# Kernel tuning notes

Measured on AMD Instinct MI355X. Metric: run time of the kernel, lower is better.

## Reference

```python
import jax, jax.numpy as jnp
import numpy as np

N_NODES = 50000


def gcn_conv(h, W, b, src, dst, n_nodes):
    # PyG GCNConv: h' = D^{-1/2} (A + I) D^{-1/2} (h @ W) + b
    h = h @ W  # [N, out]
    deg = jax.ops.segment_sum(jnp.ones_like(dst, dtype=h.dtype), dst, num_segments=n_nodes)
    dinv = jnp.where(deg > 0, jax.lax.rsqrt(deg), 0.0)  # [N]
    norm = dinv[src] * dinv[dst]  # [E]
    msg = h[src] * norm[:, None]  # [E, out]
    out = jax.ops.segment_sum(msg, dst, num_segments=n_nodes)
    return out + b


def setup_inputs() -> dict:
    key = jax.random.key(0)
    ks = jax.random.split(key, 12)
    N, E, P, D, H = N_NODES, 1600000, 200000, 128, 128
    s = lambda fan_in: 1.0 / np.sqrt(fan_in)
    return {
        "x": jax.random.normal(ks[0], (N, D), dtype=jnp.float32),
        "edge_index": jax.random.randint(ks[1], (2, E), 0, N, dtype=jnp.int32),
        "drug_pairs": jax.random.randint(ks[2], (P, 2), 0, N, dtype=jnp.int32),
        "W1": jax.random.normal(ks[3], (D, H), dtype=jnp.float32) * s(D),
        "b1": jnp.zeros((H,), dtype=jnp.float32),
        "W2": jax.random.normal(ks[4], (H, H), dtype=jnp.float32) * s(H),
        "b2": jnp.zeros((H,), dtype=jnp.float32),
        "Wh1": jax.random.normal(ks[5], (2 * H, H), dtype=jnp.float32) * s(2 * H),
        "bh1": jnp.zeros((H,), dtype=jnp.float32),
        "Wh2": jax.random.normal(ks[6], (H, 1), dtype=jnp.float32) * s(H),
        "bh2": jnp.zeros((1,), dtype=jnp.float32),
    }


def reference(x, edge_index, drug_pairs, W1, b1, W2, b2, Wh1, bh1, Wh2, bh2):
    n = x.shape[0]
    # add self-loops once (GCNConv default add_self_loops=True)
    loop = jnp.arange(n, dtype=edge_index.dtype)
    src = jnp.concatenate([edge_index[0], loop])
    dst = jnp.concatenate([edge_index[1], loop])

    h = jax.nn.relu(gcn_conv(x, W1, b1, src, dst, n))  # dropout = identity (eval)
    h = jax.nn.relu(gcn_conv(h, W2, b2, src, dst, n))

    combined = jnp.concatenate([h[drug_pairs[:, 0]], h[drug_pairs[:, 1]]], axis=1)  # [P, 2H]
    out = jax.nn.relu(combined @ Wh1 + bh1) @ Wh2 + bh2  # [P, 1]
    return out
```

## Files before the change

### kernel.cpp

```cpp
#include <hip/hip_runtime.h>
#include <hip/hip_fp16.h>


#define BSH 9
#define BSZ (1 << BSH)
#define MSB 4096
#define XPAD 132

typedef __attribute__((ext_vector_type(8))) short bf16x8;
typedef __attribute__((ext_vector_type(4))) float f32x4;

__device__ __forceinline__ float4 h4_to_f4(uint2 u) {
  float2 fa = __half22float2(*(__half2*)&u.x);
  float2 fb = __half22float2(*(__half2*)&u.y);
  return make_float4(fa.x, fa.y, fb.x, fb.y);
}

__global__ __launch_bounds__(256) void k_zero_i32(int* __restrict__ p, int n) {
  int i = blockIdx.x * 256 + threadIdx.x;
  if (i < n) p[i] = 0;
}

__global__ __launch_bounds__(256) void k_bucket_hist(const int* __restrict__ dst,
                                                     int* __restrict__ gcnt,
                                                     int e, int kb) {
  __shared__ int h[128];
  int tid = threadIdx.x;
  if (tid < kb) h[tid] = 0;
  __syncthreads();
  int stride = gridDim.x * 256;
  for (int i = blockIdx.x * 256 + tid; i < e; i += stride) {
    int d = __builtin_nontemporal_load(&dst[i]);
    atomicAdd(&h[d >> BSH], 1);
  }
  __syncthreads();
  if (tid < kb) atomicAdd(&gcnt[tid], h[tid]);
}

__global__ __launch_bounds__(128) void k_bucket_scan(const int* __restrict__ gcnt,
                                                     int* __restrict__ gbase,
                                                     int* __restrict__ gcur,
                                                     int kb) {
  __shared__ int ws[2];
  int t = threadIdx.x;
  int lane = t & 63, w = t >> 6;
  int v = (t < kb) ? gcnt[t] : 0;
  int orig = v;
#pragma unroll
  for (int o = 1; o < 64; o <<= 1) {
    int u = __shfl_up(v, o, 64);
    if (lane >= o) v += u;
  }
  if (lane == 63) ws[w] = v;
  __syncthreads();
  int ex = ((w == 1) ? ws[0] : 0) + v - orig;
  if (t < kb) { gbase[t] = ex; gcur[t] = ex; }
  if (t == kb - 1) gbase[kb] = ex + orig;
}

__global__ __launch_bounds__(256) void k_multisplit(const int* __restrict__ src,
                                                    const int* __restrict__ dst,
                                                    int* __restrict__ gcur,
                                                    int* __restrict__ tmp,
                                                    int e, int kb) {
  __shared__ int h[128], base[128];
  int tid = threadIdx.x;
  if (tid < kb) h[tid] = 0;
  __syncthreads();
  int i0 = blockIdx.x * MSB + tid;
  int d[16], rk[16];
#pragma unroll
  for (int u = 0; u < 16; ++u) {
    int i = i0 + u * 256;
    if (i < e) {
      d[u] = __builtin_nontemporal_load(&dst[i]);
      rk[u] = atomicAdd(&h[d[u] >> BSH], 1);
    }
  }
  __syncthreads();
  if (tid < kb && h[tid] > 0) base[tid] = atomicAdd(&gcur[tid], h[tid]);
  __syncthreads();
#pragma unroll
  for (int u = 0; u < 16; ++u) {
    int i = i0 + u * 256;
    if (i < e) {
      int s = __builtin_nontemporal_load(&src[i]);
      tmp[base[d[u] >> BSH] + rk[u]] = ((d[u] & (BSZ - 1)) << 16) | s;
    }
  }
}

__global__ __launch_bounds__(512) void k_bucket_build(
    const int* __restrict__ tmp, const int* __restrict__ gbase,
    int* __restrict__ rowptr, float* __restrict__ dinv,
    unsigned short* __restrict__ colarr, int n, int kb, int e) {
  __shared__ int dl[BSZ], cl[BSZ], ws[8];
  int t = threadIdx.x, b = blockIdx.x;
  int s0 = gbase[b], s1 = gbase[b + 1];
  dl[t] = 0;
  __syncthreads();
  for (int j = s0 + t; j < s1; j += 512)
    atomicAdd(&dl[((unsigned)tmp[j]) >> 16], 1);
  __syncthreads();
  int lane = t & 63, w = t >> 6;
  int v = dl[t], orig = v;
#pragma unroll
  for (int o = 1; o < 64; o <<= 1) {
    int u = __shfl_up(v, o, 64);
    if (lane >= o) v += u;
  }
  if (lane == 63) ws[w] = v;
  __syncthreads();
  if (t == 0) {
    int a = 0;
#pragma unroll
    for (int k = 0; k < 8; ++k) { int x = ws[k]; ws[k] = a; a += x; }
  }
  __syncthreads();
  int ex = ws[w] + v - orig;
  cl[t] = ex;
  int node = (b << BSH) + t;
  if (node < n) {
    rowptr[node] = s0 + ex;
    dinv[node] = rsqrtf((float)(orig + 1));
  }
  if (b == kb - 1 && t == 0) rowptr[n] = e;
  __syncthreads();
  for (int j = s0 + t; j < s1; j += 512) {
    int p = tmp[j];
    int r = atomicAdd(&cl[((unsigned)p) >> 16], 1);
    colarr[s0 + r] = (unsigned short)(p & 0xFFFF);
  }
}

__device__ __forceinline__ void split8(const float* v, bf16x8& hi, bf16x8& lo) {
#pragma unroll
  for (int j = 0; j < 8; ++j) {
    unsigned u = __float_as_uint(v[j]);
    hi[j] = (short)(u >> 16);
    float lf = v[j] - __uint_as_float(u & 0xffff0000u);
    lo[j] = (short)(__float_as_uint(lf) >> 16);
  }
}

__global__ __launch_bounds__(256) void k_prep_w(
    const float* __restrict__ W1, const float* __restrict__ W2,
    const float* __restrict__ Wh1, short* __restrict__ fragH,
    short* __restrict__ fragL) {
  int g = blockIdx.x * 256 + threadIdx.x;
  if (g >= 4 * 2048) return;
  int w = g >> 11;
  int rem = g & 2047;
  int lane = rem & 63;
  int ts = rem >> 6;
  int t = ts >> 2, s = ts & 3;
  int n = (t << 4) + (lane & 15);
  int k0 = s * 32 + (lane >> 4) * 8;
  const float* W = (w == 0) ? W1 : (w == 1) ? W2 : (w == 2) ? Wh1 : (Wh1 + 128 * 128);
  short h[8], l[8];
#pragma unroll
  for (int j = 0; j < 8; ++j) {
    float x = W[(k0 + j) * 128 + n];
    unsigned u = __float_as_uint(x);
    h[j] = (short)(u >> 16);
    float lf = x - __uint_as_float(u & 0xffff0000u);
    l[j] = (short)(__float_as_uint(lf) >> 16);
  }
  ((int4*)fragH)[g] = *(int4*)h;
  ((int4*)fragL)[g] = *(int4*)l;
}

__global__ __launch_bounds__(256) void k_gemm_mfma(
    const float* __restrict__ X, const short* __restrict__ fragH,
    const short* __restrict__ fragL, const float* __restrict__ rowscale,
    __half* __restrict__ C16, int n) {
  __shared__ float sX[64 * XPAD];
  int tid = threadIdx.x;
  int row0 = blockIdx.x * 64;
  const float2* X2 = (const float2*)(X + (size_t)row0 * 128);
#pragma unroll
  for (int it = 0; it < 16; ++it) {
    int t = it * 256 + tid;
    int r = t >> 6, c2 = t & 63;
    int gr = row0 + r;
    float2 v = (gr < n) ? X2[t] : make_float2(0.f, 0.f);
    *(float2*)&sX[r * XPAD + c2 * 2] = v;
  }
  __syncthreads();
  int wid = tid >> 6, lane = tid & 63;
  int r0 = row0 + wid * 16;
  if (r0 >= n) return;
  int m = lane & 15, quad = lane >> 4;
  const float* xrow = sX + (wid * 16 + m) * XPAD;
  f32x4 acc[8];
#pragma unroll
  for (int t = 0; t < 8; ++t) acc[t] = (f32x4)(0.f);
  const int4* FH = (const int4*)fragH;
  const int4* FL = (const int4*)fragL;
#pragma unroll
  for (int s = 0; s < 4; ++s) {
    int k0 = s * 32 + quad * 8;
    float xv[8];
    *(float2*)&xv[0] = *(const float2*)(xrow + k0);
    *(float2*)&xv[2] = *(const float2*)(xrow + k0 + 2);
    *(float2*)&xv[4] = *(const float2*)(xrow + k0 + 4);
    *(float2*)&xv[6] = *(const float2*)(xrow + k0 + 6);
    bf16x8 ah, al;
    split8(xv, ah, al);
#pragma unroll
    for (int t = 0; t < 8; ++t) {
      int idx = (t * 4 + s) * 64 + lane;
      bf16x8 bh = *(const bf16x8*)&FH[idx];
      bf16x8 bl = *(const bf16x8*)&FL[idx];
      acc[t] = __builtin_amdgcn_mfma_f32_16x16x32_bf16(ah, bh, acc[t], 0, 0, 0);
      acc[t] = __builtin_amdgcn_mfma_f32_16x16x32_bf16(al, bh, acc[t], 0, 0, 0);
      acc[t] = __builtin_amdgcn_mfma_f32_16x16x32_bf16(ah, bl, acc[t], 0, 0, 0);
    }
  }
  float sc[4];
#pragma unroll
  for (int r = 0; r < 4; ++r)
    sc[r] = rowscale ? rowscale[r0 + quad * 4 + r] : 1.f;
#pragma unroll
  for (int t = 0; t < 8; ++t) {
#pragma unroll
    for (int r = 0; r < 4; ++r) {
      int row = r0 + quad * 4 + r;
      C16[(size_t)row * 128 + t * 16 + m] = __float2half(acc[t][r] * sc[r]);
    }
  }
}

__global__ __launch_bounds__(256) void k_gemm_dual(
    const float* __restrict__ X,
    const short* __restrict__ fHa, const short* __restrict__ fLa,
    const short* __restrict__ fHb, const short* __restrict__ fLb,
    __half* __restrict__ A16, __half* __restrict__ B16, int n) {
  __shared__ float sX[64 * XPAD];
  int tid = threadIdx.x;
  int row0 = blockIdx.x * 64;
  const float2* X2 = (const float2*)(X + (size_t)row0 * 128);
#pragma unroll
  for (int it = 0; it < 16; ++it) {
    int t = it * 256 + tid;
    int r = t >> 6, c2 = t & 63;
    int gr = row0 + r;
    float2 v = (gr < n) ? X2[t] : make_float2(0.f, 0.f);
    *(float2*)&sX[r * XPAD + c2 * 2] = v;
  }
  __syncthreads();
  int wid = tid >> 6, lane = tid & 63;
  int r0 = row0 + wid * 16;
  if (r0 >= n) return;
  int m = lane & 15, quad = lane >> 4;
  const float* xrow = sX + (wid * 16 + m) * XPAD;
  f32x4 accA[8], accB[8];
#pragma unroll
  for (int t = 0; t < 8; ++t) { accA[t] = (f32x4)(0.f); accB[t] = (f32x4)(0.f); }
  const int4* FHa = (const int4*)fHa; const int4* FLa = (const int4*)fLa;
  const int4* FHb = (const int4*)fHb; const int4* FLb = (const int4*)fLb;
#pragma unroll
  for (int s = 0; s < 4; ++s) {
    int k0 = s * 32 + quad * 8;
    float xv[8];
    *(float2*)&xv[0] = *(const float2*)(xrow + k0);
    *(float2*)&xv[2] = *(const float2*)(xrow + k0 + 2);
    *(float2*)&xv[4] = *(const float2*)(xrow + k0 + 4);
    *(float2*)&xv[6] = *(const float2*)(xrow + k0 + 6);
    bf16x8 ah, al;
    split8(xv, ah, al);
#pragma unroll
    for (int t = 0; t < 8; ++t) {
      int idx = (t * 4 + s) * 64 + lane;
      bf16x8 bha = *(const bf16x8*)&FHa[idx];
      bf16x8 bla = *(const bf16x8*)&FLa[idx];
      accA[t] = __builtin_amdgcn_mfma_f32_16x16x32_bf16(ah, bha, accA[t], 0, 0, 0);
      accA[t] = __builtin_amdgcn_mfma_f32_16x16x32_bf16(al, bha, accA[t], 0, 0, 0);
      accA[t] = __builtin_amdgcn_mfma_f32_16x16x32_bf16(ah, bla, accA[t], 0, 0, 0);
      bf16x8 bhb = *(const bf16x8*)&FHb[idx];
      bf16x8 blb = *(const bf16x8*)&FLb[idx];
      accB[t] = __builtin_amdgcn_mfma_f32_16x16x32_bf16(ah, bhb, accB[t], 0, 0, 0);
      accB[t] = __builtin_amdgcn_mfma_f32_16x16x32_bf16(al, bhb, accB[t], 0, 0, 0);
      accB[t] = __builtin_amdgcn_mfma_f32_16x16x32_bf16(ah, blb, accB[t], 0, 0, 0);
    }
  }
#pragma unroll
  for (int t = 0; t < 8; ++t) {
#pragma unroll
    for (int r = 0; r < 4; ++r) {
      int row = r0 + quad * 4 + r;
      A16[(size_t)row * 128 + t * 16 + m] = __float2half(accA[t][r]);
      B16[(size_t)row * 128 + t * 16 + m] = __float2half(accB[t][r]);
    }
  }
}

__global__ __launch_bounds__(256) void k_agg_h(
    const __half2* __restrict__ g2, const float* __restrict__ dinv,
    const int* __restrict__ rowptr, const unsigned short* __restrict__ col,
    const float* __restrict__ bias, float* __restrict__ out, int n) {
  int i = blockIdx.x * 4 + (threadIdx.x >> 6);
  if (i >= n) return;
  int lane = threadIdx.x & 63;
  int sub = lane >> 5;
  int c4 = lane & 31;
  const uint2* G4 = (const uint2*)g2;
  float4 a0 = make_float4(0.f, 0.f, 0.f, 0.f), a1 = a0, a2 = a0, a3 = a0;
  if (sub == 0) a0 = h4_to_f4(G4[(size_t)i * 32 + c4]);
  int beg = rowptr[i], end = rowptr[i + 1];
  int j = beg;
  for (; j + 8 <= end; j += 8) {
    int s0 = __builtin_nontemporal_load(&col[j + 0 + sub]);
    int s1 = __builtin_nontemporal_load(&col[j + 2 + sub]);
    int s2 = __builtin_nontemporal_load(&col[j + 4 + sub]);
    int s3 = __builtin_nontemporal_load(&col[j + 6 + sub]);
    float4 v0 = h4_to_f4(G4[(size_t)s0 * 32 + c4]);
    float4 v1 = h4_to_f4(G4[(size_t)s1 * 32 + c4]);
    float4 v2 = h4_to_f4(G4[(size_t)s2 * 32 + c4]);
    float4 v3 = h4_to_f4(G4[(size_t)s3 * 32 + c4]);
    a0.x += v0.x; a0.y += v0.y; a0.z += v0.z; a0.w += v0.w;
    a1.x += v1.x; a1.y += v1.y; a1.z += v1.z; a1.w += v1.w;
    a2.x += v2.x; a2.y += v2.y; a2.z += v2.z; a2.w += v2.w;
    a3.x += v3.x; a3.y += v3.y; a3.z += v3.z; a3.w += v3.w;
  }
  for (; j + 2 <= end; j += 2) {
    int s0 = __builtin_nontemporal_load(&col[j + sub]);
    float4 v = h4_to_f4(G4[(size_t)s0 * 32 + c4]);
    a0.x += v.x; a0.y += v.y; a0.z += v.z; a0.w += v.w;
  }
  if (j < end && sub == 0) {
    int s0 = __builtin_nontemporal_load(&col[j]);
    float4 v = h4_to_f4(G4[(size_t)s0 * 32 + c4]);
    a0.x += v.x; a0.y += v.y; a0.z += v.z; a0.w += v.w;
  }
  float4 s;
  s.x = (a0.x + a1.x) + (a2.x + a3.x);
  s.y = (a0.y + a1.y) + (a2.y + a3.y);
  s.z = (a0.z + a1.z) + (a2.z + a3.z);
  s.w = (a0.w + a1.w) + (a2.w + a3.w);
  s.x += __shfl_down(s.x, 32, 64);
  s.y += __shfl_down(s.y, 32, 64);
  s.z += __shfl_down(s.z, 32, 64);
  s.w += __shfl_down(s.w, 32, 64);
  if (sub == 0) {
    float di = dinv[i];
    float4 bi = ((const float4*)bias)[c4];
    float4 o;
    o.x = fmaxf(fmaf(di, s.x, bi.x), 0.f);
    o.y = fmaxf(fmaf(di, s.y, bi.y), 0.f);
    o.z = fmaxf(fmaf(di, s.z, bi.z), 0.f);
    o.w = fmaxf(fmaf(di, s.w, bi.w), 0.f);
    ((float4*)out)[(size_t)i * 32 + c4] = o;
  }
}

__global__ __launch_bounds__(256) void k_pairs_h(
    const __half2* __restrict__ A, const __half2* __restrict__ B,
    const int* __restrict__ pairs, const float* __restrict__ bh1,
    const float* __restrict__ wh2, const float* __restrict__ bh2,
    float* __restrict__ out, int P) {
  int p = blockIdx.x * 4 + (threadIdx.x >> 6);
  int lane = threadIdx.x & 63;
  if (p >= P) return;
  int sub = lane >> 5, c4 = lane & 31;
  int p0 = pairs[2 * p], p1 = pairs[2 * p + 1];
  const uint2* T4 = sub ? (const uint2*)B : (const uint2*)A;
  int row = sub ? p1 : p0;
  float4 v = h4_to_f4(T4[(size_t)row * 32 + c4]);
  v.x += __shfl_xor(v.x, 32, 64);
  v.y += __shfl_xor(v.y, 32, 64);
  v.z += __shfl_xor(v.z, 32, 64);
  v.w += __shfl_xor(v.w, 32, 64);
  float4 bi = ((const float4*)bh1)[c4];
  float4 wv = ((const float4*)wh2)[c4];
  float s = fmaxf(v.x + bi.x, 0.f) * wv.x + fmaxf(v.y + bi.y, 0.f) * wv.y +
            fmaxf(v.z + bi.z, 0.f) * wv.z + fmaxf(v.w + bi.w, 0.f) * wv.w;
#pragma unroll
  for (int o = 16; o > 0; o >>= 1) s += __shfl_down(s, o, 64);
  if (lane == 0) out[p] = s + bh2[0];
}

extern "C" void kernel_launch(void* const* d_in, const int* in_sizes, int n_in,
                              void* d_out, int out_size, void* d_ws, size_t ws_size,
                              hipStream_t stream) {
  const float* x   = (const float*)d_in[0];
  const int* ei    = (const int*)d_in[1];
  const int* pairs = (const int*)d_in[2];
  const float* W1  = (const float*)d_in[3];
  const float* b1  = (const float*)d_in[4];
  const float* W2  = (const float*)d_in[5];
  const float* b2  = (const float*)d_in[6];
  const float* Wh1 = (const float*)d_in[7];
  const float* bh1 = (const float*)d_in[8];
  const float* Wh2 = (const float*)d_in[9];
  const float* bh2 = (const float*)d_in[10];
  (void)n_in; (void)out_size; (void)ws_size;

  int N = in_sizes[0] / 128;
  int E = in_sizes[1] / 2;
  int P = in_sizes[2] / 2;
  const int* src = ei;
  const int* dst = ei + E;
  int KB = (N + BSZ - 1) >> BSH;

  char* wsp = (char*)d_ws;
  size_t off = 0;
  auto alloc = [&](size_t bytes) -> void* {
    void* p = wsp + off;
    off += (bytes + 255) & ~(size_t)255;
    return p;
  };
  __half* g16 = (__half*)alloc((size_t)N * 128 * 2);
  float* h1   = (float*)alloc((size_t)N * 128 * 4);
  float* h2   = (float*)alloc((size_t)N * 128 * 4);
  float* dinv = (float*)alloc((size_t)N * 4);
  int* rowptr = (int*)alloc((size_t)(N + 1) * 4);
  unsigned short* colarr = (unsigned short*)alloc((size_t)E * 2);
  int* tmp    = (int*)alloc((size_t)E * 4);
  short* fragH = (short*)alloc(4 * 2048 * 8 * 2);
  short* fragL = (short*)alloc(4 * 2048 * 8 * 2);
  int* gcnt  = (int*)alloc((size_t)(KB + 1) * 4);
  int* gbase = (int*)alloc((size_t)(KB + 1) * 4);
  int* gcur  = (int*)alloc((size_t)(KB + 1) * 4);
  __half* A16 = g16;
  __half* B16 = (__half*)h1;
  short* fH_W1 = fragH + 0 * 16384;  short* fL_W1 = fragL + 0 * 16384;
  short* fH_W2 = fragH + 1 * 16384;  short* fL_W2 = fragL + 1 * 16384;
  short* fH_Wa = fragH + 2 * 16384;  short* fL_Wa = fragL + 2 * 16384;
  short* fH_Wb = fragH + 3 * 16384;  short* fL_Wb = fragL + 3 * 16384;

  k_prep_w<<<32, 256, 0, stream>>>(W1, W2, Wh1, fragH, fragL);

  k_zero_i32<<<1, 256, 0, stream>>>(gcnt, KB + 1);
  k_bucket_hist<<<256, 256, 0, stream>>>(dst, gcnt, E, KB);
  k_bucket_scan<<<1, 128, 0, stream>>>(gcnt, gbase, gcur, KB);
  k_multisplit<<<(E + MSB - 1) / MSB, 256, 0, stream>>>(src, dst, gcur, tmp, E, KB);
  k_bucket_build<<<KB, 512, 0, stream>>>(tmp, gbase, rowptr, dinv, colarr, N, KB, E);

  int GB = (N + 63) / 64;
  int AB = (N + 3) / 4;
  k_gemm_mfma<<<GB, 256, 0, stream>>>(x, fH_W1, fL_W1, dinv, g16, N);
  k_agg_h<<<AB, 256, 0, stream>>>((const __half2*)g16, dinv, rowptr, colarr, b1, h1, N);
  k_gemm_mfma<<<GB, 256, 0, stream>>>(h1, fH_W2, fL_W2, dinv, g16, N);
  k_agg_h<<<AB, 256, 0, stream>>>((const __half2*)g16, dinv, rowptr, colarr, b2, h2, N);
  k_gemm_dual<<<GB, 256, 0, stream>>>(h2, fH_Wa, fL_Wa, fH_Wb, fL_Wb, A16, B16, N);
  k_pairs_h<<<(P + 3) / 4, 256, 0, stream>>>((const __half2*)A16, (const __half2*)B16,
                                             pairs, bh1, Wh2, bh2, (float*)d_out, P);
}
```

Baseline: 385.5 us.

## Fold CSR build launches, per-wave histograms, and widen aggregation loads to 16B

After: 377.2 us. -2.2%, faster.

```diff
diff --git a/kernel.cpp b/kernel.cpp
--- a/kernel.cpp
+++ b/kernel.cpp
@@ -6,131 +6,24 @@
 #define BSZ (1 << BSH)
 #define MSB 4096
 #define XPAD 132
+#define HB 256
 
 typedef __attribute__((ext_vector_type(8))) short bf16x8;
 typedef __attribute__((ext_vector_type(4))) float f32x4;
+
+__device__ __forceinline__ void acc8(uint4 u, float4& lo, float4& hi) {
+  float2 f0 = __half22float2(((const __half2*)&u)[0]);
+  float2 f1 = __half22float2(((const __half2*)&u)[1]);
+  float2 f2 = __half22float2(((const __half2*)&u)[2]);
+  float2 f3 = __half22float2(((const __half2*)&u)[3]);
+  lo.x += f0.x; lo.y += f0.y; lo.z += f1.x; lo.w += f1.y;
+  hi.x += f2.x; hi.y += f2.y; hi.z += f3.x; hi.w += f3.y;
+}
 
 __device__ __forceinline__ float4 h4_to_f4(uint2 u) {
   float2 fa = __half22float2(*(__half2*)&u.x);
   float2 fb = __half22float2(*(__half2*)&u.y);
   return make_float4(fa.x, fa.y, fb.x, fb.y);
-}
-
-__global__ __launch_bounds__(256) void k_zero_i32(int* __restrict__ p, int n) {
-  int i = blockIdx.x * 256 + threadIdx.x;
-  if (i < n) p[i] = 0;
-}
-
-__global__ __launch_bounds__(256) void k_bucket_hist(const int* __restrict__ dst,
-                                                     int* __restrict__ gcnt,
-                                                     int e, int kb) {
-  __shared__ int h[128];
-  int tid = threadIdx.x;
-  if (tid < kb) h[tid] = 0;
-  __syncthreads();
-  int stride = gridDim.x * 256;
-  for (int i = blockIdx.x * 256 + tid; i < e; i += stride) {
-    int d = __builtin_nontemporal_load(&dst[i]);
-    atomicAdd(&h[d >> BSH], 1);
-  }
-  __syncthreads();
-  if (tid < kb) atomicAdd(&gcnt[tid], h[tid]);
-}
-
-__global__ __launch_bounds__(128) void k_bucket_scan(const int* __restrict__ gcnt,
-                                                     int* __restrict__ gbase,
-                                                     int* __restrict__ gcur,
-                                                     int kb) {
-  __shared__ int ws[2];
-  int t = threadIdx.x;
-  int lane = t & 63, w = t >> 6;
-  int v = (t < kb) ? gcnt[t] : 0;
-  int orig = v;
-#pragma unroll
-  for (int o = 1; o < 64; o <<= 1) {
-    int u = __shfl_up(v, o, 64);
-    if (lane >= o) v += u;
-  }
-  if (lane == 63) ws[w] = v;
-  __syncthreads();
-  int ex = ((w == 1) ? ws[0] : 0) + v - orig;
-  if (t < kb) { gbase[t] = ex; gcur[t] = ex; }
-  if (t == kb - 1) gbase[kb] = ex + orig;
-}
-
-__global__ __launch_bounds__(256) void k_multisplit(const int* __restrict__ src,
-                                                    const int* __restrict__ dst,
-                                                    int* __restrict__ gcur,
-                                                    int* __restrict__ tmp,
-                                                    int e, int kb) {
-  __shared__ int h[128], base[128];
-  int tid = threadIdx.x;
-  if (tid < kb) h[tid] = 0;
-  __syncthreads();
-  int i0 = blockIdx.x * MSB + tid;
-  int d[16], rk[16];
-#pragma unroll
-  for (int u = 0; u < 16; ++u) {
-    int i = i0 + u * 256;
-    if (i < e) {
-      d[u] = __builtin_nontemporal_load(&dst[i]);
-      rk[u] = atomicAdd(&h[d[u] >> BSH], 1);
-    }
-  }
-  __syncthreads();
-  if (tid < kb && h[tid] > 0) base[tid] = atomicAdd(&gcur[tid], h[tid]);
-  __syncthreads();
-#pragma unroll
-  for (int u = 0; u < 16; ++u) {
-    int i = i0 + u * 256;
-    if (i < e) {
-      int s = __builtin_nontemporal_load(&src[i]);
-      tmp[base[d[u] >> BSH] + rk[u]] = ((d[u] & (BSZ - 1)) << 16) | s;
-    }
-  }
-}
-
-__global__ __launch_bounds__(512) void k_bucket_build(
-    const int* __restrict__ tmp, const int* __restrict__ gbase,
-    int* __restrict__ rowptr, float* __restrict__ dinv,
-    unsigned short* __restrict__ colarr, int n, int kb, int e) {
-  __shared__ int dl[BSZ], cl[BSZ], ws[8];
-  int t = threadIdx.x, b = blockIdx.x;
-  int s0 = gbase[b], s1 = gbase[b + 1];
-  dl[t] = 0;
-  __syncthreads();
-  for (int j = s0 + t; j < s1; j += 512)
-    atomicAdd(&dl[((unsigned)tmp[j]) >> 16], 1);
-  __syncthreads();
-  int lane = t & 63, w = t >> 6;
-  int v = dl[t], orig = v;
-#pragma unroll
-  for (int o = 1; o < 64; o <<= 1) {
-    int u = __shfl_up(v, o, 64);
-    if (lane >= o) v += u;
-  }
-  if (lane == 63) ws[w] = v;
-  __syncthreads();
-  if (t == 0) {
-    int a = 0;
-#pragma unroll
-    for (int k = 0; k < 8; ++k) { int x = ws[k]; ws[k] = a; a += x; }
-  }
-  __syncthreads();
-  int ex = ws[w] + v - orig;
-  cl[t] = ex;
-  int node = (b << BSH) + t;
-  if (node < n) {
-    rowptr[node] = s0 + ex;
-    dinv[node] = rsqrtf((float)(orig + 1));
-  }
-  if (b == kb - 1 && t == 0) rowptr[n] = e;
-  __syncthreads();
-  for (int j = s0 + t; j < s1; j += 512) {
-    int p = tmp[j];
-    int r = atomicAdd(&cl[((unsigned)p) >> 16], 1);
-    colarr[s0 + r] = (unsigned short)(p & 0xFFFF);
-  }
 }
 
 __device__ __forceinline__ void split8(const float* v, bf16x8& hi, bf16x8& lo) {
@@ -146,9 +39,14 @@
 __global__ __launch_bounds__(256) void k_prep_w(
     const float* __restrict__ W1, const float* __restrict__ W2,
     const float* __restrict__ Wh1, short* __restrict__ fragH,
-    short* __restrict__ fragL) {
+    short* __restrict__ fragL, int* __restrict__ gcnt, int* __restrict__ gcur,
+    int kb) {
+  if (blockIdx.x == 32) {
+    int t = threadIdx.x;
+    if (t < kb) { gcnt[t] = 0; gcur[t] = 0; }
+    return;
+  }
   int g = blockIdx.x * 256 + threadIdx.x;
-  if (g >= 4 * 2048) return;
   int w = g >> 11;
   int rem = g & 2047;
   int lane = rem & 63;
@@ -170,13 +68,28 @@
   ((int4*)fragL)[g] = *(int4*)l;
 }
 
-__global__ __launch_bounds__(256) void k_gemm_mfma(
+__global__ __launch_bounds__(256) void k_hist(const int* __restrict__ dst,
+                                              int* __restrict__ gcnt,
+                                              int e, int kb) {
+  __shared__ int h4[512];
+  int tid = threadIdx.x, wid = tid >> 6;
+  for (int t = tid; t < 512; t += 256) h4[t] = 0;
+  __syncthreads();
+  for (int i = blockIdx.x * 256 + tid; i < e; i += HB * 256) {
+    int d = __builtin_nontemporal_load(&dst[i]);
+    atomicAdd(&h4[wid * 128 + (d >> BSH)], 1);
+  }
+  __syncthreads();
+  if (tid < kb)
+    atomicAdd(&gcnt[tid], h4[tid] + h4[128 + tid] + h4[256 + tid] + h4[384 + tid]);
+}
+
+__device__ __forceinline__ void gemm_body(
     const float* __restrict__ X, const short* __restrict__ fragH,
     const short* __restrict__ fragL, const float* __restrict__ rowscale,
-    __half* __restrict__ C16, int n) {
-  __shared__ float sX[64 * XPAD];
+    __half* __restrict__ C16, int n, int bid, float* sX) {
   int tid = threadIdx.x;
-  int row0 = blockIdx.x * 64;
+  int row0 = bid * 64;
   const float2* X2 = (const float2*)(X + (size_t)row0 * 128);
 #pragma unroll
   for (int it = 0; it < 16; ++it) {
@@ -228,6 +141,120 @@
       int row = r0 + quad * 4 + r;
       C16[(size_t)row * 128 + t * 16 + m] = __float2half(acc[t][r] * sc[r]);
     }
+  }
+}
+
+__global__ __launch_bounds__(256) void k_gemm_mfma(
+    const float* __restrict__ X, const short* __restrict__ fragH,
+    const short* __restrict__ fragL, const float* __restrict__ rowscale,
+    __half* __restrict__ C16, int n) {
+  __shared__ float sX[64 * XPAD];
+  gemm_body(X, fragH, fragL, rowscale, C16, n, blockIdx.x, sX);
+}
+
+__global__ __launch_bounds__(256) void k_multisplit(const int* __restrict__ src,
+                                                    const int* __restrict__ dst,
+                                                    const int* __restrict__ gcnt,
+                                                    int* __restrict__ gcur,
+                                                    int* __restrict__ tmp,
+                                                    int e, int kb) {
+  __shared__ int h4[4 * 128], off[4 * 128], sbase[128], ws[2];
+  int tid = threadIdx.x, wid = tid >> 6, lane = tid & 63;
+  for (int t = tid; t < 512; t += 256) h4[t] = 0;
+  __syncthreads();
+  int i0 = blockIdx.x * MSB + tid;
+  int d[16], rk[16];
+#pragma unroll
+  for (int u = 0; u < 16; ++u) {
+    int i = i0 + u * 256;
+    if (i < e) {
+      d[u] = __builtin_nontemporal_load(&dst[i]);
+      rk[u] = atomicAdd(&h4[wid * 128 + (d[u] >> BSH)], 1);
+    }
+  }
+  __syncthreads();
+  int tot = 0;
+  if (tid < 128) {
+    int c0 = h4[tid], c1 = h4[128 + tid], c2 = h4[256 + tid], c3 = h4[384 + tid];
+    off[tid] = 0; off[128 + tid] = c0;
+    off[256 + tid] = c0 + c1; off[384 + tid] = c0 + c1 + c2;
+    tot = c0 + c1 + c2 + c3;
+  }
+  int v = (tid < 128 && tid < kb) ? gcnt[tid] : 0;
+  int orig = v;
+#pragma unroll
+  for (int o = 1; o < 64; o <<= 1) {
+    int u = __shfl_up(v, o, 64);
+    if (lane >= o) v += u;
+  }
+  if (lane == 63 && wid < 2) ws[wid] = v;
+  __syncthreads();
+  if (tid < 128) sbase[tid] = ((wid == 1) ? ws[0] : 0) + v - orig;
+  __syncthreads();
+  if (tid < kb && tot > 0) sbase[tid] += atomicAdd(&gcur[tid], tot);
+  __syncthreads();
+#pragma unroll
+  for (int u = 0; u < 16; ++u) {
+    int i = i0 + u * 256;
+    if (i < e) {
+      int s = __builtin_nontemporal_load(&src[i]);
+      int k = d[u] >> BSH;
+      tmp[sbase[k] + off[wid * 128 + k] + rk[u]] = ((d[u] & (BSZ - 1)) << 16) | s;
+    }
+  }
+}
+
+__global__ __launch_bounds__(512) void k_bucket_build(
+    const int* __restrict__ tmp, const int* __restrict__ gcnt,
+    int* __restrict__ rowptr, float* __restrict__ dinv,
+    unsigned short* __restrict__ colarr, int n, int kb, int e) {
+  __shared__ int dl[BSZ], cl[BSZ], sbase[128], ws[8];
+  int t = threadIdx.x, b = blockIdx.x;
+  int lane = t & 63, w = t >> 6;
+  int v = (t < 128 && t < kb) ? gcnt[t] : 0;
+  int orig0 = v;
+#pragma unroll
+  for (int o = 1; o < 64; o <<= 1) {
+    int u = __shfl_up(v, o, 64);
+    if (lane >= o) v += u;
+  }
+  if (lane == 63 && w < 2) ws[w] = v;
+  dl[t] = 0;
+  __syncthreads();
+  if (t < 128) sbase[t] = ((w == 1) ? ws[0] : 0) + v - orig0;
+  __syncthreads();
+  int s0 = sbase[b];
+  int s1 = s0 + gcnt[b];
+  for (int j = s0 + t; j < s1; j += 512)
+    atomicAdd(&dl[((unsigned)tmp[j]) >> 16], 1);
+  __syncthreads();
+  int dv = dl[t], orig = dv;
+#pragma unroll
+  for (int o = 1; o < 64; o <<= 1) {
+    int u = __shfl_up(dv, o, 64);
+    if (lane >= o) dv += u;
+  }
+  if (lane == 63) ws[w] = dv;
+  __syncthreads();
+  if (t == 0) {
+    int a = 0;
+#pragma unroll
+    for (int k = 0; k < 8; ++k) { int x = ws[k]; ws[k] = a; a += x; }
+  }
+  __syncthreads();
+  int ex = ws[w] + dv - orig;
+  cl[t] = ex;
+  int node = (b << BSH) + t;
+  if (node < n) {
+    rowptr[node] = s0 + ex;
+    dinv[node] = rsqrtf((float)(orig + 1));
+  }
+  if (b == kb - 1 && t == 0) rowptr[n] = e;
+  __syncthreads();
+  for (int j = s0 + t; j < s1; j += 512) {
+    int p = tmp[j];
+    int r = atomicAdd(&cl[((unsigned)p) >> 16], 1);
+    colarr[s0 + r] = (unsigned short)(p & 0xFFFF);
   }
 }
 
@@ -302,55 +329,67 @@
   int i = blockIdx.x * 4 + (threadIdx.x >> 6);
   if (i >= n) return;
   int lane = threadIdx.x & 63;
-  int sub = lane >> 5;
-  int c4 = lane & 31;
-  const uint2* G4 = (const uint2*)g2;
-  float4 a0 = make_float4(0.f, 0.f, 0.f, 0.f), a1 = a0, a2 = a0, a3 = a0;
-  if (sub == 0) a0 = h4_to_f4(G4[(size_t)i * 32 + c4]);
+  int sub = lane >> 4;
+  int c8 = lane & 15;
+  const uint4* G = (const uint4*)g2;
+  float4 z = make_float4(0.f, 0.f, 0.f, 0.f);
+  float4 lo0 = z, lo1 = z, lo2 = z, lo3 = z, hi0 = z, hi1 = z, hi2 = z, hi3 = z;
+  if (sub == 0) acc8(G[(size_t)i * 16 + c8], lo0, hi0);
   int beg = rowptr[i], end = rowptr[i + 1];
   int j = beg;
-  for (; j + 8 <= end; j += 8) {
-    int s0 = __builtin_nontemporal_load(&col[j + 0 + sub]);
-    int s1 = __builtin_nontemporal_load(&col[j + 2 + sub]);
-    int s2 = __builtin_nontemporal_load(&col[j + 4 + sub]);
-    int s3 = __builtin_nontemporal_load(&col[j + 6 + sub]);
-    float4 v0 = h4_to_f4(G4[(size_t)s0 * 32 + c4]);
-    float4 v1 = h4_to_f4(G4[(size_t)s1 * 32 + c4]);
-    float4 v2 = h4_to_f4(G4[(size_t)s2 * 32 + c4]);
-    float4 v3 = h4_to_f4(G4[(size_t)s3 * 32 + c4]);
-    a0.x += v0.x; a0.y += v0.y; a0.z += v0.z; a0.w += v0.w;
-    a1.x += v1.x; a1.y += v1.y; a1.z += v1.z; a1.w += v1.w;
-    a2.x += v2.x; a2.y += v2.y; a2.z += v2.z; a2.w += v2.w;
-    a3.x += v3.x; a3.y += v3.y; a3.z += v3.z; a3.w += v3.w;
-  }
-  for (; j + 2 <= end; j += 2) {
+  for (; j + 16 <= end; j += 16) {
     int s0 = __builtin_nontemporal_load(&col[j + sub]);
-    float4 v = h4_to_f4(G4[(size_t)s0 * 32 + c4]);
-    a0.x += v.x; a0.y += v.y; a0.z += v.z; a0.w += v.w;
-  }
-  if (j < end && sub == 0) {
-    int s0 = __builtin_nontemporal_load(&col[j]);
-    float4 v = h4_to_f4(G4[(size_t)s0 * 32 + c4]);
-    a0.x += v.x; a0.y += v.y; a0.z += v.z; a0.w += v.w;
-  }
-  float4 s;
-  s.x = (a0.x + a1.x) + (a2.x + a3.x);
-  s.y = (a0.y + a1.y) + (a2.y + a3.y);
-  s.z = (a0.z + a1.z) + (a2.z + a3.z);
-  s.w = (a0.w + a1.w) + (a2.w + a3.w);
-  s.x += __shfl_down(s.x, 32, 64);
-  s.y += __shfl_down(s.y, 32, 64);
-  s.z += __shfl_down(s.z, 32, 64);
-  s.w += __shfl_down(s.w, 32, 64);
+    int s1 = __builtin_nontemporal_load(&col[j + 4 + sub]);
+    int s2 = __builtin_nontemporal_load(&col[j + 8 + sub]);
+    int s3 = __builtin_nontemporal_load(&col[j + 12 + sub]);
+    uint4 u0 = G[(size_t)s0 * 16 + c8];
+    uint4 u1 = G[(size_t)s1 * 16 + c8];
+    uint4 u2 = G[(size_t)s2 * 16 + c8];
+    uint4 u3 = G[(size_t)s3 * 16 + c8];
+    acc8(u0, lo0, hi0); acc8(u1, lo1, hi1);
+    acc8(u2, lo2, hi2); acc8(u3, lo3, hi3);
+  }
+  for (; j + 4 <= end; j += 4) {
+    int s0 = __builtin_nontemporal_load(&col[j + sub]);
+    acc8(G[(size_t)s0 * 16 + c8], lo1, hi1);
+  }
+  int rem = end - j;
+  if (sub < rem) {
+    int s0 = __builtin_nontemporal_load(&col[j + sub]);
+    acc8(G[(size_t)s0 * 16 + c8], lo2, hi2);
+  }
+  float4 lo, hi;
+  lo.x = (lo0.x + lo1.x) + (lo2.x + lo3.x);
+  lo.y = (lo0.y + lo1.y) + (lo2.y + lo3.y);
+  lo.z = (lo0.z + lo1.z) + (lo2.z + lo3.z);
+  lo.w = (lo0.w + lo1.w) + (lo2.w + lo3.w);
+  hi.x = (hi0.x + hi1.x) + (hi2.x + hi3.x);
+  hi.y = (hi0.y + hi1.y) + (hi2.y + hi3.y);
+  hi.z = (hi0.z + hi1.z) + (hi2.z + hi3.z);
+  hi.w = (hi0.w + hi1.w) + (hi2.w + hi3.w);
+  lo.x += __shfl_down(lo.x, 32, 64); lo.x += __shfl_down(lo.x, 16, 64);
+  lo.y += __shfl_down(lo.y, 32, 64); lo.y += __shfl_down(lo.y, 16, 64);
+  lo.z += __shfl_down(lo.z, 32, 64); lo.z += __shfl_down(lo.z, 16, 64);
+  lo.w += __shfl_down(lo.w, 32, 64); lo.w += __shfl_down(lo.w, 16, 64);
+  hi.x += __shfl_down(hi.x, 32, 64); hi.x += __shfl_down(hi.x, 16, 64);
+  hi.y += __shfl_down(hi.y, 32, 64); hi.y += __shfl_down(hi.y, 16, 64);
+  hi.z += __shfl_down(hi.z, 32, 64); hi.z += __shfl_down(hi.z, 16, 64);
+  hi.w += __shfl_down(hi.w, 32, 64); hi.w += __shfl_down(hi.w, 16, 64);
   if (sub == 0) {
     float di = dinv[i];
-    float4 bi = ((const float4*)bias)[c4];
-    float4 o;
-    o.x = fmaxf(fmaf(di, s.x, bi.x), 0.f);
-    o.y = fmaxf(fmaf(di, s.y, bi.y), 0.f);
-    o.z = fmaxf(fmaf(di, s.z, bi.z), 0.f);
-    o.w = fmaxf(fmaf(di, s.w, bi.w), 0.f);
-    ((float4*)out)[(size_t)i * 32 + c4] = o;
+    float4 b0 = ((const float4*)bias)[2 * c8];
+    float4 b1 = ((const float4*)bias)[2 * c8 + 1];
+    float4 o0, o1;
+    o0.x = fmaxf(fmaf(di, lo.x, b0.x), 0.f);
+    o0.y = fmaxf(fmaf(di, lo.y, b0.y), 0.f);
+    o0.z = fmaxf(fmaf(di, lo.z, b0.z), 0.f);
+    o0.w = fmaxf(fmaf(di, lo.w, b0.w), 0.f);
+    o1.x = fmaxf(fmaf(di, hi.x, b1.x), 0.f);
+    o1.y = fmaxf(fmaf(di, hi.y, b1.y), 0.f);
+    o1.z = fmaxf(fmaf(di, hi.z, b1.z), 0.f);
+    o1.w = fmaxf(fmaf(di, hi.w, b1.w), 0.f);
+    ((float4*)out)[(size_t)i * 32 + 2 * c8] = o0;
+    ((float4*)out)[(size_t)i * 32 + 2 * c8 + 1] = o1;
   }
 }
 
@@ -420,7 +459,6 @@
   short* fragH = (short*)alloc(4 * 2048 * 8 * 2);
   short* fragL = (short*)alloc(4 * 2048 * 8 * 2);
   int* gcnt  = (int*)alloc((size_t)(KB + 1) * 4);
-  int* gbase = (int*)alloc((size_t)(KB + 1) * 4);
   int* gcur  = (int*)alloc((size_t)(KB + 1) * 4);
   __half* A16 = g16;
   __half* B16 = (__half*)h1;
@@ -429,16 +467,14 @@
   short* fH_Wa = fragH + 2 * 16384;  short* fL_Wa = fragL + 2 * 16384;
   short* fH_Wb = fragH + 3 * 16384;  short* fL_Wb = fragL + 3 * 16384;
 
-  k_prep_w<<<32, 256, 0, stream>>>(W1, W2, Wh1, fragH, fragL);
-
-  k_zero_i32<<<1, 256, 0, stream>>>(gcnt, KB + 1);
-  k_bucket_hist<<<256, 256, 0, stream>>>(dst, gcnt, E, KB);
-  k_bucket_scan<<<1, 128, 0, stream>>>(gcnt, gbase, gcur, KB);
-  k_multisplit<<<(E + MSB - 1) / MSB, 256, 0, stream>>>(src, dst, gcur, tmp, E, KB);
-  k_bucket_build<<<KB, 512, 0, stream>>>(tmp, gbase, rowptr, dinv, colarr, N, KB, E);
-
   int GB = (N + 63) / 64;
   int AB = (N + 3) / 4;
+
+  k_prep_w<<<33, 256, 0, stream>>>(W1, W2, Wh1, fragH, fragL, gcnt, gcur, KB);
+  k_hist<<<HB, 256, 0, stream>>>(dst, gcnt, E, KB);
+  k_multisplit<<<(E + MSB - 1) / MSB, 256, 0, stream>>>(src, dst, gcnt, gcur,
+                                                        tmp, E, KB);
+  k_bucket_build<<<KB, 512, 0, stream>>>(tmp, gcnt, rowptr, dinv, colarr, N, KB, E);
   k_gemm_mfma<<<GB, 256, 0, stream>>>(x, fH_W1, fL_W1, dinv, g16, N);
   k_agg_h<<<AB, 256, 0, stream>>>((const __half2*)g16, dinv, rowptr, colarr, b1, h1, N);
   k_gemm_mfma<<<GB, 256, 0, stream>>>(h1, fH_W2, fL_W2, dinv, g16, N);
```
